# Kernel tuning notes

Hardware: AMD Instinct MI355X
Metric: run time of the kernel (lower is better)

Reference implementation:

```python
import jax, jax.numpy as jnp
import numpy as np

L, E, NH, V, BS = 8, 1024, 16, 32000, 1024  # layers, embed, heads, vocab, block_size
HD = E // NH  # head dim = 64
FF = 4 * E


def layernorm(x, scale, bias, eps=1e-5):
    mu = jnp.mean(x, axis=-1, keepdims=True)
    var = jnp.var(x, axis=-1, keepdims=True)
    return (x - mu) * jax.lax.rsqrt(var + eps) * scale + bias


def setup_inputs() -> dict:
    key = jax.random.key(0)
    ks = jax.random.split(key, 16)
    s = 0.02
    B, T = 2, 1024
    return {
        "idx": jax.random.randint(ks[0], (B, T), 0, V),
        "tok_emb": jax.random.normal(ks[1], (V, E), jnp.float32) * s,
        "pos_emb": jax.random.normal(ks[2], (BS, E), jnp.float32) * s,
        "Wq": jax.random.normal(ks[3], (L, E, E), jnp.float32) * s,
        "Wk": jax.random.normal(ks[4], (L, E, E), jnp.float32) * s,
        "Wv": jax.random.normal(ks[5], (L, E, E), jnp.float32) * s,
        "Wo": jax.random.normal(ks[6], (L, E, E), jnp.float32) * s,
        "bo": jnp.zeros((L, E), jnp.float32),
        "ln1_s": jnp.ones((L, E), jnp.float32),
        "ln1_b": jnp.zeros((L, E), jnp.float32),
        "W1": jax.random.normal(ks[7], (L, E, FF), jnp.float32) * s,
        "b1": jnp.zeros((L, FF), jnp.float32),
        "W2": jax.random.normal(ks[8], (L, FF, E), jnp.float32) * s,
        "b2": jnp.zeros((L, E), jnp.float32),
        "ln2_s": jnp.ones((L, E), jnp.float32),
        "ln2_b": jnp.zeros((L, E), jnp.float32),
        "lnf_s": jnp.ones((E,), jnp.float32),
        "lnf_b": jnp.zeros((E,), jnp.float32),
        "lm_w": jax.random.normal(ks[9], (E, V), jnp.float32) * s,
        "lm_b": jnp.zeros((V,), jnp.float32),
    }


def reference(idx, tok_emb, pos_emb, Wq, Wk, Wv, Wo, bo, ln1_s, ln1_b,
              W1, b1, W2, b2, ln2_s, ln2_b, lnf_s, lnf_b, lm_w, lm_b):
    B, T = idx.shape
    x = tok_emb[idx] + pos_emb[:T]  # [B,T,E]
    causal = jnp.triu(jnp.ones((T, T), bool), 1)  # True above diagonal -> masked
    scale = 1.0 / jnp.sqrt(jnp.asarray(HD, x.dtype))
    for l in range(L):
        h = layernorm(x, ln1_s[l], ln1_b[l])
        q = (h @ Wq[l]).reshape(B, T, NH, HD)
        k = (h @ Wk[l]).reshape(B, T, NH, HD)
        v = (h @ Wv[l]).reshape(B, T, NH, HD)
        scores = jnp.einsum("bthd,bshd->bhts", q, k) * scale  # [B,H,T,T]
        scores = jnp.where(causal, -jnp.inf, scores)
        attn = jax.nn.softmax(scores, axis=-1)
        o = jnp.einsum("bhts,bshd->bthd", attn, v).reshape(B, T, E)
        x = x + o @ Wo[l] + bo[l]
        h2 = layernorm(x, ln2_s[l], ln2_b[l])
        x = x + jax.nn.gelu(h2 @ W1[l] + b1[l], approximate=False) @ W2[l] + b2[l]
    x = layernorm(x, lnf_s, lnf_b)
    logits = x @ lm_w + lm_b  # [B,T,V]
    return logits
```

## Files before the change

kernel.cpp:

```cpp
#include <hip/hip_runtime.h>

#define EDIM 1024
#define NHEADS 16
#define HDIM 64
#define TSEQ 1024
#define NBATCH 2
#define MROWS 2048
#define FFDIM 4096
#define NLAYERS 8
#define VOCAB 32000
#define QKVN 3072
#define SC2 0.18033688011112042f

typedef __attribute__((ext_vector_type(4))) float f32x4;
typedef __attribute__((ext_vector_type(8))) short short8;

__device__ __forceinline__ unsigned short f2bf(float f) {
    union { float f; unsigned u; } v; v.f = f;
    unsigned r = v.u + 0x7fffu + ((v.u >> 16) & 1u);
    return (unsigned short)(r >> 16);
}

__device__ __forceinline__ float bf2f(unsigned u) {
    union { unsigned u; float f; } v; v.u = u << 16; return v.f;
}

__device__ __forceinline__ f32x4 mfma_bf16(short8 a, short8 b, f32x4 c) {
    return __builtin_amdgcn_mfma_f32_16x16x32_bf16(a, b, c, 0, 0, 0);
}

__device__ __forceinline__ void gload16(const unsigned short* g, unsigned short* l) {
    __builtin_amdgcn_global_load_lds(
        (const __attribute__((address_space(1))) unsigned int*)g,
        (__attribute__((address_space(3))) unsigned int*)l, 16, 0, 0);
}

__device__ __forceinline__ void ln_store(
    f32x4 v, int tid, const float* __restrict__ sc, const float* __restrict__ bi,
    unsigned short* __restrict__ hrow)
{
    float sum = v[0] + v[1] + v[2] + v[3];
    float sq = v[0]*v[0] + v[1]*v[1] + v[2]*v[2] + v[3]*v[3];
    #pragma unroll
    for (int m = 1; m <= 32; m <<= 1) { sum += __shfl_xor(sum, m); sq += __shfl_xor(sq, m); }
    __shared__ float sh[8];
    int w = tid >> 6;
    if ((tid & 63) == 0) { sh[w] = sum; sh[4 + w] = sq; }
    __syncthreads();
    sum = sh[0] + sh[1] + sh[2] + sh[3];
    sq  = sh[4] + sh[5] + sh[6] + sh[7];
    float mu = sum * (1.0f / EDIM);
    float inv = rsqrtf(sq * (1.0f / EDIM) - mu * mu + 1e-5f);
    int c = tid * 4;
    unsigned o0 = (unsigned)f2bf((v[0] - mu) * inv * sc[c + 0] + bi[c + 0])
                | ((unsigned)f2bf((v[1] - mu) * inv * sc[c + 1] + bi[c + 1]) << 16);
    unsigned o1 = (unsigned)f2bf((v[2] - mu) * inv * sc[c + 2] + bi[c + 2])
                | ((unsigned)f2bf((v[3] - mu) * inv * sc[c + 3] + bi[c + 3]) << 16);
    unsigned* hp = (unsigned*)(hrow + c);
    hp[0] = o0; hp[1] = o1;
}

__global__ __launch_bounds__(256) void embed_ln_kernel(
    const int* __restrict__ idx, const float* __restrict__ tok,
    const float* __restrict__ pos, float* __restrict__ x,
    const float* __restrict__ sc, const float* __restrict__ bi,
    unsigned short* __restrict__ h)
{
    int row = blockIdx.x, tid = threadIdx.x;
    int t = row & (TSEQ - 1);
    int tokid = idx[row];
    int c = tid * 4;
    f32x4 a = *(const f32x4*)(tok + (size_t)tokid * EDIM + c);
    f32x4 b = *(const f32x4*)(pos + (size_t)t * EDIM + c);
    f32x4 v = a + b;
    *(f32x4*)(x + (size_t)row * EDIM + c) = v;
    ln_store(v, tid, sc, bi, h + (size_t)row * EDIM);
}

template<int KZ>
__global__ __launch_bounds__(256) void reduce_ln_kernel(
    const unsigned short* __restrict__ part, const float* __restrict__ bias,
    float* __restrict__ x, const float* __restrict__ sc,
    const float* __restrict__ bi, unsigned short* __restrict__ h)
{
    int row = blockIdx.x, tid = threadIdx.x;
    int c = tid * 4;
    f32x4 s = *(const f32x4*)(x + (size_t)row * EDIM + c);
    s += *(const f32x4*)(bias + c);
    #pragma unroll
    for (int kz = 0; kz < KZ; ++kz) {
        const unsigned* p = (const unsigned*)(part + ((size_t)kz * MROWS + row) * EDIM + c);
        unsigned p0 = p[0], p1 = p[1];
        s[0] += bf2f(p0); s[1] += bf2f(p0 >> 16);
        s[2] += bf2f(p1); s[3] += bf2f(p1 >> 16);
    }
    *(f32x4*)(x + (size_t)row * EDIM + c) = s;
    ln_store(s, tid, sc, bi, h + (size_t)row * EDIM);
}

__device__ __forceinline__ void conv_tile(
    unsigned short* __restrict__ Tb,
    const float* __restrict__ W, unsigned short* __restrict__ WT,
    int Kdim, int Ndim, int k0, int n0, int tid)
{
    int r = tid >> 4, c4 = (tid & 15) * 4;
    #pragma unroll
    for (int i = 0; i < 4; ++i) {
        f32x4 v = *(const f32x4*)(W + (size_t)(k0 + r + 16 * i) * Ndim + n0 + c4);
        Tb[(c4 + 0) * 72 + r + 16 * i] = f2bf(v[0]);
        Tb[(c4 + 1) * 72 + r + 16 * i] = f2bf(v[1]);
        Tb[(c4 + 2) * 72 + r + 16 * i] = f2bf(v[2]);
        Tb[(c4 + 3) * 72 + r + 16 * i] = f2bf(v[3]);
    }
    __syncthreads();
    int nr = tid >> 2, kc = (tid & 3) * 16;
    short8 o0 = *(const short8*)&Tb[nr * 72 + kc];
    short8 o1 = *(const short8*)&Tb[nr * 72 + kc + 8];
    *(short8*)(WT + (size_t)(n0 + nr) * Kdim + k0 + kc)     = o0;
    *(short8*)(WT + (size_t)(n0 + nr) * Kdim + k0 + kc + 8) = o1;
}

__device__ __forceinline__ void wconv_layer_body(
    unsigned short* Tb, int t, int tid,
    const float* Wq, const float* Wk, const float* Wv, const float* Wo,
    const float* W1, const float* W2,
    unsigned short* qkvT, unsigned short* woT,
    unsigned short* w1T, unsigned short* w2T)
{
    if (t < 768) {
        int wsel = t >> 8, tt = t & 255;
        const float* src = wsel == 0 ? Wq : (wsel == 1 ? Wk : Wv);
        conv_tile(Tb, src, qkvT + (size_t)wsel * EDIM * EDIM, EDIM, EDIM,
                  (tt & 15) * 64, (tt >> 4) * 64, tid);
    } else if (t < 1024) {
        int tt = t - 768;
        conv_tile(Tb, Wo, woT, EDIM, EDIM, (tt & 15) * 64, (tt >> 4) * 64, tid);
    } else if (t < 2048) {
        int tt = t - 1024;
        conv_tile(Tb, W1, w1T, EDIM, FFDIM, (tt & 15) * 64, (tt >> 4) * 64, tid);
    } else {
        int tt = t - 2048;
        conv_tile(Tb, W2, w2T, FFDIM, EDIM, (tt >> 4) * 64, (tt & 15) * 64, tid);
    }
}

__global__ __launch_bounds__(256) void wconv_layer_kernel(
    const float* __restrict__ Wq, const float* __restrict__ Wk,
    const float* __restrict__ Wv, const float* __restrict__ Wo,
    const float* __restrict__ W1, const float* __restrict__ W2,
    unsigned short* __restrict__ qkvT, unsigned short* __restrict__ woT,
    unsigned short* __restrict__ w1T, unsigned short* __restrict__ w2T)
{
    __shared__ __align__(16) unsigned short Tb[64 * 72];
    wconv_layer_body(Tb, blockIdx.x, threadIdx.x, Wq, Wk, Wv, Wo, W1, W2,
                     qkvT, woT, w1T, w2T);
}

__global__ __launch_bounds__(256) void wconv_kernel(
    const float* __restrict__ W, unsigned short* __restrict__ WT, int Kdim, int Ndim)
{
    __shared__ __align__(16) unsigned short Tb[64 * 72];
    conv_tile(Tb, W, WT, Kdim, Ndim, blockIdx.x * 64, blockIdx.y * 64, threadIdx.x);
}

template<int EPI>
__device__ __forceinline__ void gemm128_body(
    unsigned short* SMEM,
    const unsigned short* __restrict__ A, const unsigned short* __restrict__ WT,
    unsigned short* __restrict__ Cb,
    int Ndim, int Kdim, int ntiles, int nwg, int kspan, int bid, int kz)
{
    unsigned short* A_lds = SMEM;
    unsigned short* B_lds = SMEM + 8192;
    int tid = threadIdx.x;
    int q8 = nwg >> 3;
    int swz = (bid & 7) * q8 + (bid >> 3);
    int bm0 = (swz / ntiles) * 128, bn0 = (swz % ntiles) * 128;
    int lane = tid & 63, w = tid >> 6;
    int wr = w >> 1, wc = w & 1;
    int r16 = lane & 15, cc = lane >> 4;
    int lrow = lane >> 3;
    int lcol = ((lane & 7) ^ lrow) * 8;
    int sw = r16 & 7;

    f32x4 acc[4][4];
    #pragma unroll
    for (int m = 0; m < 4; ++m)
        #pragma unroll
        for (int n = 0; n < 4; ++n) acc[m][n] = {0.f, 0.f, 0.f, 0.f};

    int kbeg = kz * kspan, kend = kbeg + kspan;
    for (int k0 = kbeg; k0 < kend; k0 += 64) {
        #pragma unroll
        for (int i = 0; i < 4; ++i) {
            int c = i * 4 + w;
            gload16(A + (size_t)(bm0 + c * 8 + lrow) * Kdim + k0 + lcol, A_lds + c * 512);
            gload16(WT + (size_t)(bn0 + c * 8 + lrow) * Kdim + k0 + lcol, B_lds + c * 512);
        }
        __syncthreads();
        #pragma unroll
        for (int kh = 0; kh < 2; ++kh) {
            short8 af[4], bfr[4];
            #pragma unroll
            for (int m = 0; m < 4; ++m)
                af[m] = *(const short8*)&A_lds[(wr * 64 + m * 16 + r16) * 64 + ((kh * 4 + cc) ^ sw) * 8];
            #pragma unroll
            for (int n = 0; n < 4; ++n)
                bfr[n] = *(const short8*)&B_lds[(wc * 64 + n * 16 + r16) * 64 + ((kh * 4 + cc) ^ sw) * 8];
            #pragma unroll
            for (int m = 0; m < 4; ++m)
                #pragma unroll
                for (int n = 0; n < 4; ++n)
                    acc[m][n] = mfma_bf16(af[m], bfr[n], acc[m][n]);
        }
        __syncthreads();
    }

    #pragma unroll
    for (int m = 0; m < 4; ++m) {
        #pragma unroll
        for (int n = 0; n < 4; ++n) {
            #pragma unroll
            for (int j = 0; j < 4; ++j) {
                int row = bm0 + wr * 64 + m * 16 + cc * 4 + j;
                int col = bn0 + wc * 64 + n * 16 + r16;
                float vv = acc[m][n][j];
                if constexpr (EPI == 0)
                    Cb[(size_t)row * Ndim + col] = f2bf(vv);
                else
                    Cb[((size_t)kz * MROWS + row) * Ndim + col] = f2bf(vv);
            }
        }
    }
}

template<int EPI>
__global__ __launch_bounds__(256, 3) void gemm128(
    const unsigned short* __restrict__ A, const unsigned short* __restrict__ WT,
    unsigned short* __restrict__ Cb,
    int Ndim, int Kdim, int ntiles, int nwg, int kspan)
{
    __shared__ __align__(16) unsigned short SMEM[16384];
    gemm128_body<EPI>(SMEM, A, WT, Cb, Ndim, Kdim, ntiles, nwg, kspan,
                      blockIdx.x, blockIdx.y);
}

template<int MODE>
__global__ __launch_bounds__(256, 3) void ff2_fused_kernel(
    const unsigned short* __restrict__ A, const unsigned short* __restrict__ WT,
    unsigned short* __restrict__ Cp,
    const float* __restrict__ Wq, const float* __restrict__ Wk,
    const float* __restrict__ Wv, const float* __restrict__ Wo,
    const float* __restrict__ W1, const float* __restrict__ W2,
    const float* __restrict__ lmW,
    unsigned short* __restrict__ qkvT, unsigned short* __restrict__ woT,
    unsigned short* __restrict__ w1T, unsigned short* __restrict__ w2Tn,
    unsigned short* __restrict__ lmT)
{
    __shared__ __align__(16) unsigned short SMEM[16384];
    int bid = blockIdx.x;
    if (bid < 512) {
        gemm128_body<4>(SMEM, A, WT, Cp, EDIM, FFDIM, 8, 128, 1024,
                        bid & 127, bid >> 7);
    } else if constexpr (MODE == 0) {
        wconv_layer_body(SMEM, bid - 512, threadIdx.x, Wq, Wk, Wv, Wo, W1, W2,
                         qkvT, woT, w1T, w2Tn);
    } else {
        int t = bid - 512;
        conv_tile(SMEM, lmW, lmT, EDIM, VOCAB, (t & 15) * 64, (t >> 4) * 64, threadIdx.x);
    }
}

template<int EPI>
__global__ __launch_bounds__(512, 2) void gemm_p3(
    const unsigned short* __restrict__ A, const unsigned short* __restrict__ WT,
    const float* __restrict__ bias, float* __restrict__ Cf,
    unsigned short* __restrict__ Cb, int Ndim, int Kdim, int mtiles, int ntiles)
{
    __shared__ __align__(16) unsigned short LDS[3][24576];
    const int tid = threadIdx.x;
    const int nwg = mtiles * ntiles, q8 = nwg >> 3;
    const int swz = (int)(blockIdx.x & 7) * q8 + (int)(blockIdx.x >> 3);
    const int bn0 = (swz / mtiles) * 256, bm0 = (swz % mtiles) * 128;
    const int lane = tid & 63, w = tid >> 6;
    const int wr = w >> 2, wc = w & 3;
    const int r16 = lane & 15, cc = lane >> 4;
    const int lrow = lane >> 3;
    const int lcol = ((lane & 7) ^ lrow) * 8;
    const int sw = r16 & 7;

    f32x4 acc[4][4];
    #pragma unroll
    for (int m = 0; m < 4; ++m)
        #pragma unroll
        for (int n = 0; n < 4; ++n) acc[m][n] = {0.f, 0.f, 0.f, 0.f};

    const int nk = Kdim >> 6;

    auto STAGE = [&](int t, int bufidx) {
        int k0 = t * 64;
        unsigned short* buf = &LDS[bufidx][0];
        #pragma unroll
        for (int i = 0; i < 2; ++i) {
            int c = i * 8 + w;
            gload16(A + (size_t)(bm0 + c * 8 + lrow) * Kdim + k0 + lcol, buf + c * 512);
        }
        #pragma unroll
        for (int i = 0; i < 4; ++i) {
            int c = i * 8 + w;
            gload16(WT + (size_t)(bn0 + c * 8 + lrow) * Kdim + k0 + lcol, buf + 8192 + c * 512);
        }
    };

    STAGE(0, 0);
    STAGE(1, 1);
    asm volatile("s_waitcnt vmcnt(6)" ::: "memory");
    __builtin_amdgcn_sched_barrier(0);
    __builtin_amdgcn_s_barrier();
    __builtin_amdgcn_sched_barrier(0);

    int cur = 0;
    for (int t = 0; t < nk; ++t) {
        if (t + 2 < nk) STAGE(t + 2, cur == 0 ? 2 : cur - 1);
        const unsigned short* Abuf = &LDS[cur][0];
        const unsigned short* Bbuf = &LDS[cur][8192];
        #pragma unroll
        for (int kh = 0; kh < 2; ++kh) {
            short8 af[4], bfr[4];
            #pragma unroll
            for (int m = 0; m < 4; ++m)
                af[m] = *(const short8*)&Abuf[(wr * 64 + m * 16 + r16) * 64 + ((kh * 4 + cc) ^ sw) * 8];
            #pragma unroll
            for (int n = 0; n < 4; ++n)
                bfr[n] = *(const short8*)&Bbuf[(wc * 64 + n * 16 + r16) * 64 + ((kh * 4 + cc) ^ sw) * 8];
            __builtin_amdgcn_s_setprio(1);
            #pragma unroll
            for (int m = 0; m < 4; ++m)
                #pragma unroll
                for (int n = 0; n < 4; ++n)
                    acc[m][n] = mfma_bf16(af[m], bfr[n], acc[m][n]);
            __builtin_amdgcn_s_setprio(0);
        }
        if (t + 1 < nk) {
            if (t + 2 < nk) asm volatile("s_waitcnt vmcnt(6)" ::: "memory");
            else            asm volatile("s_waitcnt vmcnt(0)" ::: "memory");
            __builtin_amdgcn_sched_barrier(0);
            __builtin_amdgcn_s_barrier();
            __builtin_amdgcn_sched_barrier(0);
            asm volatile("" ::: "memory");
        }
        cur = cur == 2 ? 0 : cur + 1;
    }

    #pragma unroll
    for (int m = 0; m < 4; ++m) {
        #pragma unroll
        for (int n = 0; n < 4; ++n) {
            #pragma unroll
            for (int j = 0; j < 4; ++j) {
                int row = bm0 + wr * 64 + m * 16 + cc * 4 + j;
                int col = bn0 + wc * 64 + n * 16 + r16;
                float vv = acc[m][n][j] + bias[col];
                if constexpr (EPI == 2) {
                    vv = 0.5f * vv * (1.0f + erff(vv * 0.70710678118654752f));
                    Cb[(size_t)row * Ndim + col] = f2bf(vv);
                } else {
                    Cf[(size_t)row * Ndim + col] = vv;
                }
            }
        }
    }
}

__global__ __launch_bounds__(256, 2) void gemm_wide_lm(
    const unsigned short* __restrict__ A, const unsigned short* __restrict__ WT,
    const float* __restrict__ bias, float* __restrict__ Cf,
    int Ndim, int Kdim, int mtiles, int ntiles)
{
    __shared__ __align__(16) unsigned short A_lds[128][64];
    __shared__ __align__(16) unsigned short B_lds[256][64];
    int tid = threadIdx.x;
    int nwg = mtiles * ntiles;
    int q8 = nwg >> 3;
    int swz = (int)(blockIdx.x & 7) * q8 + (int)(blockIdx.x >> 3);
    int bn0 = (swz / mtiles) * 256, bm0 = (swz % mtiles) * 128;
    int lane = tid & 63, w = tid >> 6;
    int wr = w >> 1, wc = w & 1;
    int r16 = lane & 15, cc = lane >> 4;
    int lrow = lane >> 3;
    int lcol = ((lane & 7) ^ lrow) * 8;
    int sw = r16 & 7;

    f32x4 acc[4][8];
    #pragma unroll
    for (int m = 0; m < 4; ++m)
        #pragma unroll
        for (int n = 0; n < 8; ++n) acc[m][n] = {0.f, 0.f, 0.f, 0.f};

    for (int k0 = 0; k0 < Kdim; k0 += 64) {
        #pragma unroll
        for (int i = 0; i < 4; ++i) {
            int c = i * 4 + w;
            gload16(A + (size_t)(bm0 + c * 8 + lrow) * Kdim + k0 + lcol,
                    (unsigned short*)A_lds + c * 512);
        }
        #pragma unroll
        for (int i = 0; i < 8; ++i) {
            int c = i * 4 + w;
            gload16(WT + (size_t)(bn0 + c * 8 + lrow) * Kdim + k0 + lcol,
                    (unsigned short*)B_lds + c * 512);
        }
        __syncthreads();
        #pragma unroll
        for (int kh = 0; kh < 2; ++kh) {
            short8 af[4], bfr[8];
            #pragma unroll
            for (int m = 0; m < 4; ++m)
                af[m] = *(const short8*)&A_lds[wr * 64 + m * 16 + r16][((kh * 4 + cc) ^ sw) * 8];
            #pragma unroll
            for (int n = 0; n < 8; ++n)
                bfr[n] = *(const short8*)&B_lds[wc * 128 + n * 16 + r16][((kh * 4 + cc) ^ sw) * 8];
            #pragma unroll
            for (int m = 0; m < 4; ++m)
                #pragma unroll
                for (int n = 0; n < 8; ++n)
                    acc[m][n] = mfma_bf16(af[m], bfr[n], acc[m][n]);
        }
        __syncthreads();
    }

    #pragma unroll
    for (int m = 0; m < 4; ++m) {
        #pragma unroll
        for (int n = 0; n < 8; ++n) {
            #pragma unroll
            for (int j = 0; j < 4; ++j) {
                int row = bm0 + wr * 64 + m * 16 + cc * 4 + j;
                int col = bn0 + wc * 128 + n * 16 + r16;
                Cf[(size_t)row * Ndim + col] = acc[m][n][j] + bias[col];
            }
        }
    }
}

__global__ __launch_bounds__(256) void attn_kernel(
    const unsigned short* __restrict__ qkv, unsigned short* __restrict__ o)
{
    __shared__ __align__(16) unsigned short K_lds[128][72];
    __shared__ __align__(16) unsigned short VT_lds[64][136];
    __shared__ __align__(16) unsigned short P_lds[4][16][136];

    int qt = (int)gridDim.x - 1 - (int)blockIdx.x;
    int head = blockIdx.y, bb = blockIdx.z;
    int tid = threadIdx.x, w = tid >> 6, lane = tid & 63;
    int r16 = lane & 15, cc = lane >> 4;
    size_t base = ((size_t)bb * TSEQ) * QKVN + head * HDIM;
    const unsigned short* q = qkv + base;
    const unsigned short* k = qkv + base + EDIM;
    const unsigned short* v = qkv + base + 2 * EDIM;
    size_t obase = ((size_t)bb * TSEQ) * EDIM + head * HDIM;
    int qbase = qt * 64;

    const unsigned short* qp = q + (size_t)(qbase + w * 16 + r16) * QKVN;
    short8 aq0 = *(const short8*)(qp + cc * 8);
    short8 aq1 = *(const short8*)(qp + 32 + cc * 8);

    f32x4 oacc[4];
    float m2[4], lrow[4];
    #pragma unroll
    for (int n = 0; n < 4; ++n) oacc[n] = {0.f, 0.f, 0.f, 0.f};
    #pragma unroll
    for (int j = 0; j < 4; ++j) { m2[j] = -1e30f; lrow[j] = 0.f; }

    int krow = tid >> 1, kch = (tid & 1) * 32;
    int vk2 = (tid & 63) * 2, vdb = (tid >> 6) * 16;
    int myrow = qbase + w * 16 + cc * 4;

    int nkt = (qt + 2) >> 1;
    for (int kt = 0; kt < nkt; ++kt) {
        int kbase = kt * 128;
        bool last = (kt == nkt - 1);
        bool half = last && !(qt & 1);
        if (!half || krow < 64) {
            const unsigned short* kp = k + (size_t)(kbase + krow) * QKVN + kch;
            *(short8*)&K_lds[krow][kch]      = *(const short8*)kp;
            *(short8*)&K_lds[krow][kch + 8]  = *(const short8*)(kp + 8);
            *(short8*)&K_lds[krow][kch + 16] = *(const short8*)(kp + 16);
            *(short8*)&K_lds[krow][kch + 24] = *(const short8*)(kp + 24);
        }
        if (!half || vk2 < 64) {
            const unsigned short* vp0 = v + (size_t)(kbase + vk2) * QKVN + vdb;
            short8 v0a = *(const short8*)vp0;
            short8 v0b = *(const short8*)(vp0 + 8);
            short8 v1a = *(const short8*)(vp0 + QKVN);
            short8 v1b = *(const short8*)(vp0 + QKVN + 8);
            #pragma unroll
            for (int i = 0; i < 8; ++i) {
                *(unsigned*)&VT_lds[vdb + i][vk2] =
                    (unsigned)(unsigned short)v0a[i] | ((unsigned)(unsigned short)v1a[i] << 16);
                *(unsigned*)&VT_lds[vdb + 8 + i][vk2] =
                    (unsigned)(unsigned short)v0b[i] | ((unsigned)(unsigned short)v1b[i] << 16);
            }
        }
        __syncthreads();

        f32x4 s[8];
        __builtin_amdgcn_s_setprio(1);
        #pragma unroll
        for (int n = 0; n < 4; ++n) {
            short8 bk0 = *(const short8*)&K_lds[n * 16 + r16][cc * 8];
            short8 bk1 = *(const short8*)&K_lds[n * 16 + r16][32 + cc * 8];
            f32x4 z = {0.f, 0.f, 0.f, 0.f};
            z = mfma_bf16(aq0, bk0, z);
            z = mfma_bf16(aq1, bk1, z);
            s[n] = z;
        }
        __builtin_amdgcn_s_setprio(0);
        if (!half) {
            __builtin_amdgcn_s_setprio(1);
            #pragma unroll
            for (int n = 4; n < 8; ++n) {
                short8 bk0 = *(const short8*)&K_lds[n * 16 + r16][cc * 8];
                short8 bk1 = *(const short8*)&K_lds[n * 16 + r16][32 + cc * 8];
                f32x4 z = {0.f, 0.f, 0.f, 0.f};
                z = mfma_bf16(aq0, bk0, z);
                z = mfma_bf16(aq1, bk1, z);
                s[n] = z;
            }
            __builtin_amdgcn_s_setprio(0);
        }

        if (last) {
            if (half) {
                #pragma unroll
                for (int n = 0; n < 4; ++n) {
                    int key = kbase + n * 16 + r16;
                    #pragma unroll
                    for (int j = 0; j < 4; ++j) {
                        float sv = s[n][j] * SC2;
                        if (key > myrow + j) sv = -1e30f;
                        s[n][j] = sv;
                    }
                }
            } else {
                #pragma unroll
                for (int n = 0; n < 4; ++n)
                    #pragma unroll
                    for (int j = 0; j < 4; ++j) s[n][j] *= SC2;
                #pragma unroll
                for (int n = 4; n < 8; ++n) {
                    int key = kbase + n * 16 + r16;
                    #pragma unroll
                    for (int j = 0; j < 4; ++j) {
                        float sv = s[n][j] * SC2;
                        if (key > myrow + j) sv = -1e30f;
                        s[n][j] = sv;
                    }
                }
            }
        } else {
            #pragma unroll
            for (int n = 0; n < 8; ++n)
                #pragma unroll
                for (int j = 0; j < 4; ++j) s[n][j] *= SC2;
        }

        float tmax[4];
        #pragma unroll
        for (int j = 0; j < 4; ++j) {
            float tm = fmaxf(fmaxf(s[0][j], s[1][j]), fmaxf(s[2][j], s[3][j]));
            if (!half) tm = fmaxf(tm, fmaxf(fmaxf(s[4][j], s[5][j]), fmaxf(s[6][j], s[7][j])));
            #pragma unroll
            for (int mm = 1; mm <= 8; mm <<= 1) tm = fmaxf(tm, __shfl_xor(tm, mm));
            tmax[j] = tm;
        }
        bool defer = (tmax[0] - m2[0] <= 11.5f) && (tmax[1] - m2[1] <= 11.5f)
                  && (tmax[2] - m2[2] <= 11.5f) && (tmax[3] - m2[3] <= 11.5f);
        if (!__all(defer)) {
            #pragma unroll
            for (int j = 0; j < 4; ++j) {
                float mnew = fmaxf(m2[j], tmax[j]);
                float al = exp2f(m2[j] - mnew);
                m2[j] = mnew;
                lrow[j] *= al;
                #pragma unroll
                for (int n = 0; n < 4; ++n) oacc[n][j] *= al;
            }
        }
        #pragma unroll
        for (int j = 0; j < 4; ++j) {
            float ts = 0.f;
            #pragma unroll
            for (int n = 0; n < 4; ++n) {
                float pe = exp2f(s[n][j] - m2[j]);
                s[n][j] = pe;
                ts += pe;
            }
            if (!half) {
                #pragma unroll
                for (int n = 4; n < 8; ++n) {
                    float pe = exp2f(s[n][j] - m2[j]);
                    s[n][j] = pe;
                    ts += pe;
                }
            }
            #pragma unroll
            for (int mm = 1; mm <= 8; mm <<= 1) ts += __shfl_xor(ts, mm);
            lrow[j] += ts;
        }
        #pragma unroll
        for (int n = 0; n < 4; ++n)
            #pragma unroll
            for (int j = 0; j < 4; ++j)
                P_lds[w][cc * 4 + j][n * 16 + r16] = f2bf(s[n][j]);
        if (!half) {
            #pragma unroll
            for (int n = 4; n < 8; ++n)
                #pragma unroll
                for (int j = 0; j < 4; ++j)
                    P_lds[w][cc * 4 + j][n * 16 + r16] = f2bf(s[n][j]);
        }
        short8 pa[4];
        pa[0] = *(const short8*)&P_lds[w][r16][cc * 8];
        pa[1] = *(const short8*)&P_lds[w][r16][32 + cc * 8];
        if (!half) {
            pa[2] = *(const short8*)&P_lds[w][r16][64 + cc * 8];
            pa[3] = *(const short8*)&P_lds[w][r16][96 + cc * 8];
        }
        __builtin_amdgcn_s_setprio(1);
        #pragma unroll
        for (int n = 0; n < 4; ++n) {
            #pragma unroll
            for (int qq = 0; qq < 2; ++qq) {
                short8 bv = *(const short8*)&VT_lds[n * 16 + r16][qq * 32 + cc * 8];
                oacc[n] = mfma_bf16(pa[qq], bv, oacc[n]);
            }
        }
        __builtin_amdgcn_s_setprio(0);
        if (!half) {
            __builtin_amdgcn_s_setprio(1);
            #pragma unroll
            for (int n = 0; n < 4; ++n) {
                #pragma unroll
                for (int qq = 2; qq < 4; ++qq) {
                    short8 bv = *(const short8*)&VT_lds[n * 16 + r16][qq * 32 + cc * 8];
                    oacc[n] = mfma_bf16(pa[qq], bv, oacc[n]);
                }
            }
            __builtin_amdgcn_s_setprio(0);
        }
        __syncthreads();
    }
    float rl[4];
    #pragma unroll
    for (int j = 0; j < 4; ++j) rl[j] = 1.0f / lrow[j];
    #pragma unroll
    for (int n = 0; n < 4; ++n)
        #pragma unroll
        for (int j = 0; j < 4; ++j) {
            int row = qbase + w * 16 + cc * 4 + j;
            o[obase + (size_t)row * EDIM + n * 16 + r16] = f2bf(oacc[n][j] * rl[j]);
        }
}

extern "C" void kernel_launch(void* const* d_in, const int* in_sizes, int n_in,
                              void* d_out, int out_size, void* d_ws, size_t ws_size,
                              hipStream_t stream) {
    const int*   idx     = (const int*)d_in[0];
    const float* tok_emb = (const float*)d_in[1];
    const float* pos_emb = (const float*)d_in[2];
    const float* Wq      = (const float*)d_in[3];
    const float* Wk      = (const float*)d_in[4];
    const float* Wv      = (const float*)d_in[5];
    const float* Wo      = (const float*)d_in[6];
    const float* bo      = (const float*)d_in[7];
    const float* ln1_s   = (const float*)d_in[8];
    const float* ln1_b   = (const float*)d_in[9];
    const float* W1      = (const float*)d_in[10];
    const float* b1      = (const float*)d_in[11];
    const float* W2      = (const float*)d_in[12];
    const float* b2      = (const float*)d_in[13];
    const float* ln2_s   = (const float*)d_in[14];
    const float* ln2_b   = (const float*)d_in[15];
    const float* lnf_s   = (const float*)d_in[16];
    const float* lnf_b   = (const float*)d_in[17];
    const float* lm_w    = (const float*)d_in[18];
    const float* lm_b    = (const float*)d_in[19];
    float* out = (float*)d_out;

    const size_t MB = 1 << 20;
    char* ws = (char*)d_ws;
    float*          x    = (float*)ws;
    unsigned short* h    = (unsigned short*)(ws + 8 * MB);
    unsigned short* qkv  = (unsigned short*)(ws + 12 * MB);
    unsigned short* ao   = (unsigned short*)(ws + 24 * MB);
    unsigned short* ff   = (unsigned short*)(ws + 28 * MB);
    unsigned short* qkvT = (unsigned short*)(ws + 44 * MB);
    unsigned short* woT  = (unsigned short*)(ws + 50 * MB);
    unsigned short* w1T  = (unsigned short*)(ws + 52 * MB);
    unsigned short* w2Ta = (unsigned short*)(ws + 60 * MB);
    unsigned short* lmT  = (unsigned short*)(ws + 68 * MB);

    bool tier1 = ws_size >= (size_t)140 * MB;
    bool tier2 = ws_size >= (size_t)172 * MB;
    unsigned short* w2Tb = tier1 ? (unsigned short*)(ws + 131 * MB) : w2Ta;
    unsigned short* part = (unsigned short*)(ws + (tier2 ? (size_t)139 * MB : (size_t)68 * MB));

    dim3 blk(256);
    embed_ln_kernel<<<MROWS, blk, 0, stream>>>(idx, tok_emb, pos_emb, x, ln1_s, ln1_b, h);
    wconv_layer_kernel<<<3072, blk, 0, stream>>>(Wq, Wk, Wv, Wo, W1, W2,
                                                 qkvT, woT, w1T, w2Ta);

    for (int l = 0; l < NLAYERS; ++l) {
        unsigned short* w2cur = (l & 1) ? w2Tb : w2Ta;
        unsigned short* w2nxt = ((l + 1) & 1) ? w2Tb : w2Ta;
        size_t eo1 = (size_t)(l + 1) * EDIM * EDIM;

        gemm128<0><<<dim3(384, 1), blk, 0, stream>>>(h, qkvT, qkv, QKVN, EDIM, 24, 384, EDIM);
        attn_kernel<<<dim3(TSEQ / 64, NHEADS, NBATCH), blk, 0, stream>>>(qkv, ao);
        gemm128<4><<<dim3(128, 4), blk, 0, stream>>>(ao, woT, part, EDIM, EDIM, 8, 128, 256);
        reduce_ln_kernel<4><<<MROWS, blk, 0, stream>>>(part, bo + l * EDIM, x, ln2_s + l * EDIM, ln2_b + l * EDIM, h);
        gemm_p3<2><<<dim3(256, 1), dim3(512), 0, stream>>>(h, w1T, b1 + l * FFDIM, nullptr, ff, FFDIM, EDIM, 16, 16);
        if (l < NLAYERS - 1) {
            if (tier1)
                ff2_fused_kernel<0><<<3584, blk, 0, stream>>>(
                    ff, w2cur, part,
                    Wq + eo1, Wk + eo1, Wv + eo1, Wo + eo1,
                    W1 + (size_t)(l + 1) * EDIM * FFDIM, W2 + (size_t)(l + 1) * FFDIM * EDIM,
                    nullptr, qkvT, woT, w1T, w2nxt, nullptr);
            else {
                gemm128<4><<<dim3(128, 4), blk, 0, stream>>>(ff, w2cur, part, EDIM, FFDIM, 8, 128, 1024);
                wconv_layer_kernel<<<3072, blk, 0, stream>>>(
                    Wq + eo1, Wk + eo1, Wv + eo1, Wo + eo1,
                    W1 + (size_t)(l + 1) * EDIM * FFDIM, W2 + (size_t)(l + 1) * FFDIM * EDIM,
                    qkvT, woT, w1T, w2nxt);
            }
        } else {
            if (tier2)
                ff2_fused_kernel<1><<<8512, blk, 0, stream>>>(
                    ff, w2cur, part,
                    nullptr, nullptr, nullptr, nullptr, nullptr, nullptr,
                    lm_w, nullptr, nullptr, nullptr, nullptr, lmT);
            else
                gemm128<4><<<dim3(128, 4), blk, 0, stream>>>(ff, w2cur, part, EDIM, FFDIM, 8, 128, 1024);
        }
        if (l < NLAYERS - 1)
            reduce_ln_kernel<4><<<MROWS, blk, 0, stream>>>(part, b2 + l * EDIM, x, ln1_s + (l + 1) * EDIM, ln1_b + (l + 1) * EDIM, h);
        else
            reduce_ln_kernel<4><<<MROWS, blk, 0, stream>>>(part, b2 + l * EDIM, x, lnf_s, lnf_b, h);
    }
    if (!tier2)
        wconv_kernel<<<dim3(16, 500), blk, 0, stream>>>(lm_w, lmT, EDIM, VOCAB);
    gemm_wide_lm<<<dim3(2000, 1), blk, 0, stream>>>(h, lmT, lm_b, out, VOCAB, EDIM, 16, 125);
}
```

Before: 1.427 ms.

## Fuse embed with weight conversion, fold score scale into QKV GEMM, tanh GELU

Merges the embedding+layernorm kernel with the first-layer weight conversion into one launch. Switches the QKV projection to the gemm_p3 kernel with a new epilogue that pre-scales Q columns by the softmax scale, so the attention kernel no longer multiplies scores. Replaces the exact erf GELU with a tanh approximation built on exp2f. The tanh GELU is an approximation and differs slightly from the erf reference, which risks numerical tolerance issues.

```diff
diff --git a/kernel.cpp b/kernel.cpp
--- a/kernel.cpp
+++ b/kernel.cpp
@@ -27,6 +27,14 @@
 
 __device__ __forceinline__ f32x4 mfma_bf16(short8 a, short8 b, f32x4 c) {
     return __builtin_amdgcn_mfma_f32_16x16x32_bf16(a, b, c, 0, 0, 0);
+}
+
+__device__ __forceinline__ float gelu_t(float x) {
+    float u = 0.7978845608028654f * (x + 0.044715f * x * x * x);
+    float t = exp2f(-2.885390081777927f * fabsf(u));
+    float th = (1.0f - t) / (1.0f + t);
+    th = u < 0.0f ? -th : th;
+    return 0.5f * x * (1.0f + th);
 }
 
 __device__ __forceinline__ void gload16(const unsigned short* g, unsigned short* l) {
@@ -60,23 +68,6 @@
     hp[0] = o0; hp[1] = o1;
 }
 
-__global__ __launch_bounds__(256) void embed_ln_kernel(
-    const int* __restrict__ idx, const float* __restrict__ tok,
-    const float* __restrict__ pos, float* __restrict__ x,
-    const float* __restrict__ sc, const float* __restrict__ bi,
-    unsigned short* __restrict__ h)
-{
-    int row = blockIdx.x, tid = threadIdx.x;
-    int t = row & (TSEQ - 1);
-    int tokid = idx[row];
-    int c = tid * 4;
-    f32x4 a = *(const f32x4*)(tok + (size_t)tokid * EDIM + c);
-    f32x4 b = *(const f32x4*)(pos + (size_t)t * EDIM + c);
-    f32x4 v = a + b;
-    *(f32x4*)(x + (size_t)row * EDIM + c) = v;
-    ln_store(v, tid, sc, bi, h + (size_t)row * EDIM);
-}
-
 template<int KZ>
 __global__ __launch_bounds__(256) void reduce_ln_kernel(
     const unsigned short* __restrict__ part, const float* __restrict__ bias,
@@ -163,6 +154,35 @@
     conv_tile(Tb, W, WT, Kdim, Ndim, blockIdx.x * 64, blockIdx.y * 64, threadIdx.x);
 }
 
+__global__ __launch_bounds__(256) void embed_wconv_kernel(
+    const int* __restrict__ idx, const float* __restrict__ tok,
+    const float* __restrict__ pos, float* __restrict__ x,
+    const float* __restrict__ sc, const float* __restrict__ bi,
+    unsigned short* __restrict__ h,
+    const float* __restrict__ Wq, const float* __restrict__ Wk,
+    const float* __restrict__ Wv, const float* __restrict__ Wo,
+    const float* __restrict__ W1, const float* __restrict__ W2,
+    unsigned short* __restrict__ qkvT, unsigned short* __restrict__ woT,
+    unsigned short* __restrict__ w1T, unsigned short* __restrict__ w2T)
+{
+    __shared__ __align__(16) unsigned short Tb[64 * 72];
+    int bid = blockIdx.x, tid = threadIdx.x;
+    if (bid < MROWS) {
+        int row = bid;
+        int t = row & (TSEQ - 1);
+        int tokid = idx[row];
+        int c = tid * 4;
+        f32x4 a = *(const f32x4*)(tok + (size_t)tokid * EDIM + c);
+        f32x4 b = *(const f32x4*)(pos + (size_t)t * EDIM + c);
+        f32x4 v = a + b;
+        *(f32x4*)(x + (size_t)row * EDIM + c) = v;
+        ln_store(v, tid, sc, bi, h + (size_t)row * EDIM);
+    } else {
+        wconv_layer_body(Tb, bid - MROWS, tid, Wq, Wk, Wv, Wo, W1, W2,
+                         qkvT, woT, w1T, w2T);
+    }
+}
+
 template<int EPI>
 __device__ __forceinline__ void gemm128_body(
     unsigned short* SMEM,
@@ -360,12 +380,15 @@
             for (int j = 0; j < 4; ++j) {
                 int row = bm0 + wr * 64 + m * 16 + cc * 4 + j;
                 int col = bn0 + wc * 64 + n * 16 + r16;
-                float vv = acc[m][n][j] + bias[col];
+                float vv = acc[m][n][j];
                 if constexpr (EPI == 2) {
-                    vv = 0.5f * vv * (1.0f + erff(vv * 0.70710678118654752f));
+                    vv += bias[col];
+                    Cb[(size_t)row * Ndim + col] = f2bf(gelu_t(vv));
+                } else if constexpr (EPI == 5) {
+                    if (col < EDIM) vv *= SC2;
                     Cb[(size_t)row * Ndim + col] = f2bf(vv);
                 } else {
-                    Cf[(size_t)row * Ndim + col] = vv;
+                    Cf[(size_t)row * Ndim + col] = vv + bias[col];
                 }
             }
         }
@@ -531,38 +554,16 @@
         }
 
         if (last) {
-            if (half) {
-                #pragma unroll
-                for (int n = 0; n < 4; ++n) {
+            int nlo = half ? 0 : 4;
+            #pragma unroll
+            for (int n = 0; n < 8; ++n) {
+                if (n >= nlo && n < nlo + 4) {
                     int key = kbase + n * 16 + r16;
                     #pragma unroll
-                    for (int j = 0; j < 4; ++j) {
-                        float sv = s[n][j] * SC2;
-                        if (key > myrow + j) sv = -1e30f;
-                        s[n][j] = sv;
-                    }
+                    for (int j = 0; j < 4; ++j)
+                        if (key > myrow + j) s[n][j] = -1e30f;
                 }
-            } else {
-                #pragma unroll
-                for (int n = 0; n < 4; ++n)
-                    #pragma unroll
-                    for (int j = 0; j < 4; ++j) s[n][j] *= SC2;
-                #pragma unroll
-                for (int n = 4; n < 8; ++n) {
-                    int key = kbase + n * 16 + r16;
-                    #pragma unroll
-                    for (int j = 0; j < 4; ++j) {
-                        float sv = s[n][j] * SC2;
-                        if (key > myrow + j) sv = -1e30f;
-                        s[n][j] = sv;
-                    }
-                }
-            }
-        } else {
-            #pragma unroll
-            for (int n = 0; n < 8; ++n)
-                #pragma unroll
-                for (int j = 0; j < 4; ++j) s[n][j] *= SC2;
+            }
         }
 
         float tmax[4];
@@ -707,16 +708,16 @@
     unsigned short* part = (unsigned short*)(ws + (tier2 ? (size_t)139 * MB : (size_t)68 * MB));
 
     dim3 blk(256);
-    embed_ln_kernel<<<MROWS, blk, 0, stream>>>(idx, tok_emb, pos_emb, x, ln1_s, ln1_b, h);
-    wconv_layer_kernel<<<3072, blk, 0, stream>>>(Wq, Wk, Wv, Wo, W1, W2,
-                                                 qkvT, woT, w1T, w2Ta);
+    embed_wconv_kernel<<<MROWS + 3072, blk, 0, stream>>>(
+        idx, tok_emb, pos_emb, x, ln1_s, ln1_b, h,
+        Wq, Wk, Wv, Wo, W1, W2, qkvT, woT, w1T, w2Ta);
 
     for (int l = 0; l < NLAYERS; ++l) {
         unsigned short* w2cur = (l & 1) ? w2Tb : w2Ta;
         unsigned short* w2nxt = ((l + 1) & 1) ? w2Tb : w2Ta;
         size_t eo1 = (size_t)(l + 1) * EDIM * EDIM;
 
-        gemm128<0><<<dim3(384, 1), blk, 0, stream>>>(h, qkvT, qkv, QKVN, EDIM, 24, 384, EDIM);
+        gemm_p3<5><<<dim3(192, 1), dim3(512), 0, stream>>>(h, qkvT, nullptr, nullptr, qkv, QKVN, EDIM, 16, 12);
         attn_kernel<<<dim3(TSEQ / 64, NHEADS, NBATCH), blk, 0, stream>>>(qkv, ao);
         gemm128<4><<<dim3(128, 4), blk, 0, stream>>>(ao, woT, part, EDIM, EDIM, 8, 128, 256);
         reduce_ln_kernel<4><<<MROWS, blk, 0, stream>>>(part, bo + l * EDIM, x, ln2_s + l * EDIM, ln2_b + l * EDIM, h);
```

Result: faster. 1.383 ms, median of 2 (-3.1%).
